# Performance work log

Measured on AMD Instinct MI355X. Metric: run time of the kernel, lower is better.

Reference implementation:

```python
import jax, jax.numpy as jnp
import numpy as np

N, E, F, H, C, B = 50000, 1_600_000, 128, 128, 10, 512


def setup_inputs() -> dict:
    key = jax.random.key(0)
    ks = jax.random.split(key, 12)
    inp = {
        "x": jax.random.normal(ks[0], (N, F), dtype=jnp.float32),
        "edge_index": jax.random.randint(ks[1], (2, E), 0, N, dtype=jnp.int32),
        "batch": jnp.sort(jax.random.randint(ks[2], (N,), 0, B, dtype=jnp.int32)),
        "edge_weight": jax.random.uniform(ks[3], (E,), dtype=jnp.float32),
        "W1": jax.random.normal(ks[4], (F, H), dtype=jnp.float32) * 0.05,
        "b1": jnp.zeros((H,), dtype=jnp.float32),
        "W2": jax.random.normal(ks[5], (H, H), dtype=jnp.float32) * 0.05,
        "b2": jnp.zeros((H,), dtype=jnp.float32),
        "W3": jax.random.normal(ks[6], (H, H), dtype=jnp.float32) * 0.05,
        "b3": jnp.zeros((H,), dtype=jnp.float32),
        "Wlin": jax.random.normal(ks[7], (H, C), dtype=jnp.float32) * 0.05,
        "blin": jnp.zeros((C,), dtype=jnp.float32),
    }
    return inp


def reference(x, edge_index, batch, edge_weight, W1, b1, W2, b2, W3, b3, Wlin, blin):
    n = x.shape[0]
    src, dst = edge_index[0], edge_index[1]
    loops = jnp.arange(n, dtype=src.dtype)
    src_f = jnp.concatenate([src, loops])  # edges + self-loops
    dst_f = jnp.concatenate([dst, loops])

    def make_norm(fill_value):
        # GCN symmetric normalization: D^-1/2 (A + fill*I) D^-1/2 on edge weights
        ew = jnp.concatenate([edge_weight, jnp.full((n,), fill_value, dtype=edge_weight.dtype)])
        deg = jax.ops.segment_sum(ew, dst_f, num_segments=n)
        dinv = jnp.where(deg > 0, deg ** -0.5, 0.0)
        return dinv[src_f] * ew * dinv[dst_f]

    # conv1 was built as GCNConv(in, hidden, out_channels) -> third positional arg is
    # `improved`, truthy => self-loop fill value 2.0; conv2/3 use 1.0.
    norm1 = make_norm(2.0)
    norm = make_norm(1.0)

    def gcn_conv(h, W, b, nrm):
        h = h @ W                                   # [N, H]
        msg = h[src_f] * nrm[:, None]               # [E+N, H] gather
        return jax.ops.segment_sum(msg, dst_f, num_segments=n) + b

    h = jax.nn.relu(gcn_conv(x, W1, b1, norm1))
    h = jax.nn.relu(gcn_conv(h, W2, b2, norm))
    h = gcn_conv(h, W3, b3, norm)

    # global_mean_pool over graph ids
    sums = jax.ops.segment_sum(h, batch, num_segments=B)
    cnt = jax.ops.segment_sum(jnp.ones((n,), dtype=h.dtype), batch, num_segments=B)
    pooled = sums / jnp.maximum(cnt, 1.0)[:, None]

    # dropout is identity in eval mode
    return pooled @ Wlin + blin
```

## Files before the change

### kernel.cpp

```cpp
#include <hip/hip_runtime.h>
#include <hip/hip_fp16.h>

#define F 128
#define HID 128
#define NCLS 10
#define CAP 80
#define NBIN 256
#define NPB 196
#define SCAP 7168
#define EPT 8
#define HLS 136

typedef short short8 __attribute__((ext_vector_type(8)));
typedef float float4v __attribute__((ext_vector_type(4)));
typedef float float2v __attribute__((ext_vector_type(2)));

__device__ __forceinline__ unsigned short f2bf(float f) {
    unsigned int u = __float_as_uint(f);
    unsigned int r = (u + 0x7FFFu + ((u >> 16) & 1u)) >> 16;
    return (unsigned short)r;
}
__device__ __forceinline__ float bf2f(unsigned int h) {
    return __uint_as_float(h << 16);
}
__device__ __forceinline__ unsigned char f2fp8(float a) {
    return (unsigned char)(__builtin_amdgcn_cvt_pk_fp8_f32(a, 0.f, 0, false) & 0xFF);
}

__global__ __launch_bounds__(256) void bin_prep_kernel(
    const int* __restrict__ ei, const float* __restrict__ ew,
    int* __restrict__ gcur, uint2* __restrict__ staging, int E, int nbb,
    const float* __restrict__ W1, const float* __restrict__ W2,
    const float* __restrict__ W3, const float* __restrict__ Wlin,
    const float* __restrict__ blin, const float* __restrict__ b3,
    unsigned short* __restrict__ Wp, unsigned short* __restrict__ Wp3s,
    float* __restrict__ bL) {
    __shared__ int lhist[NBIN];
    __shared__ int lscan[NBIN];
    __shared__ int lbase[NBIN];
    __shared__ uint2 lent[256 * EPT];
    int tid = threadIdx.x;

    if ((int)blockIdx.x < nbb) {
        lhist[tid] = 0;
        __syncthreads();

        unsigned int rpk[EPT];
        unsigned short rd[EPT];
        unsigned short rloc[EPT];
        int base = blockIdx.x * (256 * EPT);
#pragma unroll
        for (int i = 0; i < EPT; i++) {
            int e = base + tid + i * 256;
            if (e < E) {
                int s = ei[e];
                int d = ei[E + e];
                unsigned int q = (unsigned int)(ew[e] * 65535.0f + 0.5f);
                rpk[i] = (q << 16) | (unsigned int)s;
                rd[i] = (unsigned short)d;
                rloc[i] = (unsigned short)atomicAdd(&lhist[d / NPB], 1);
            } else {
                rpk[i] = 0u; rd[i] = 0; rloc[i] = 0xFFFF;
            }
        }
        __syncthreads();

        lscan[tid] = lhist[tid];
        __syncthreads();
        for (int off = 1; off < NBIN; off <<= 1) {
            int t = (tid >= off) ? lscan[tid - off] : 0;
            __syncthreads();
            lscan[tid] += t;
            __syncthreads();
        }
        lbase[tid] = atomicAdd(&gcur[tid], lhist[tid]);
        __syncthreads();

#pragma unroll
        for (int i = 0; i < EPT; i++) {
            if (rloc[i] != 0xFFFF) {
                int bin = (int)rd[i] / NPB;
                int slot = (lscan[bin] - lhist[bin]) + (int)rloc[i];
                lent[slot] = make_uint2(rpk[i], (unsigned int)rd[i]);
            }
        }
        __syncthreads();

        int total = lscan[NBIN - 1];
        for (int j = tid; j < total; j += 256) {
            uint2 t = lent[j];
            int bin = (int)t.y / NPB;
            int pos = lbase[bin] + (j - (lscan[bin] - lhist[bin]));
            if (pos < SCAP) staging[(size_t)bin * SCAP + pos] = t;
        }
    } else {
        int b = blockIdx.x - nbb;
        if (b < 128) {
            int widx = b >> 6;
            const float* W = (widx == 0) ? W1 : W2;
            int idx = (b & 63) * 256 + tid;
            int j = idx & 7;
            int l = (idx >> 3) & 63;
            int nt = (idx >> 9) & 7;
            int kt = idx >> 12;
            int k = kt * 32 + ((l >> 4) << 3) + j;
            int n = nt * 16 + (l & 15);
            Wp[widx * 16384 + idx] = f2bf(W[k * HID + n]);
        } else if (b < 136) {
            int idx = (b - 128) * 256 + tid;
            int j = idx & 7;
            int l = (idx >> 3) & 63;
            int kt = idx >> 9;
            int k = kt * 32 + ((l >> 4) << 3) + j;
            int n = l & 15;
            float v = 0.f;
            if (n < NCLS) {
                for (int m = 0; m < HID; m++)
                    v += W3[k * HID + m] * Wlin[m * NCLS + n];
            }
            Wp3s[idx] = f2bf(v);
        } else {
            if (tid < NCLS) {
                float bl = blin[tid];
                for (int j = 0; j < HID; j++) bl += b3[j] * Wlin[j * NCLS + tid];
                bL[tid] = bl;
            }
        }
    }
}

__global__ __launch_bounds__(1024, 8) void build_gemm1_kernel(
    const uint2* __restrict__ staging, const int* __restrict__ gcur,
    unsigned int* __restrict__ colw, int* __restrict__ cnt,
    float* __restrict__ dinv1, float* __restrict__ dinv0, int N, int nbins,
    const float* __restrict__ X, const unsigned short* __restrict__ Wp,
    unsigned char* __restrict__ Yb8) {
    __shared__ unsigned int lbuck[NPB * CAP];
    __shared__ int lcnt[NPB];
    int tid = threadIdx.x;

    if ((int)blockIdx.x < nbins) {
        int bin = blockIdx.x;
        int node0 = bin * NPB;

        for (int n = tid; n < NPB; n += 1024) lcnt[n] = 0;
        __syncthreads();

        int bcnt = gcur[bin];
        if (bcnt > SCAP) bcnt = SCAP;
        const uint2* st = staging + (size_t)bin * SCAP;
        for (int i = tid; i < bcnt; i += 1024) {
            uint2 t = st[i];
            int dl = (int)t.y - node0;
            int pos = atomicAdd(&lcnt[dl], 1);
            if (pos < CAP) lbuck[dl * CAP + pos] = t.x;
        }
        __syncthreads();

        for (int it = 0; it < NPB; it += 128) {
            int nl = it + (tid >> 3);
            int lane = tid & 7;
            if (nl < NPB) {
                int gn = node0 + nl;
                if (gn < N) {
                    int c = lcnt[nl];
                    if (c > CAP) c = CAP;
                    float s = 0.f;
                    for (int j = lane; j < c; j += 8)
                        s += (float)(lbuck[nl * CAP + j] >> 16);
                    s += __shfl_down(s, 4, 8);
                    s += __shfl_down(s, 2, 8);
                    s += __shfl_down(s, 1, 8);
                    if (lane == 0) {
                        float deg = s * (1.0f / 65535.0f);
                        cnt[gn] = c;
                        dinv1[gn] = 1.0f / sqrtf(deg + 2.0f);
                        dinv0[gn] = 1.0f / sqrtf(deg + 1.0f);
                    }
                }
            }
        }
        __syncthreads();

        int nvalid = N - node0;
        if (nvalid > NPB) nvalid = NPB;
        if (nvalid <= 0) return;
        int nslots = nvalid * (CAP / 4);
        uint4* dst4 = (uint4*)(colw + (size_t)node0 * CAP);
        const uint4* src4 = (const uint4*)lbuck;
        for (int i = tid; i < nslots; i += 1024) {
            int rowi = i / (CAP / 4);
            int slot = i - rowi * (CAP / 4);
            int c = lcnt[rowi];
            if (c > CAP) c = CAP;
            if (slot * 4 < c) dst4[i] = src4[i];
        }
    } else {
        int tile = blockIdx.x - nbins;
        int wave = tid >> 6, lane = tid & 63;
        int quad = lane >> 4, m = lane & 15;
        int row0 = tile * 256 + wave * 16;
        if (row0 >= N) return;
        int row = row0 + m;
        int rowc = row < N ? row : N - 1;

        short8 a[4];
        const float4* xrow = (const float4*)(X + (size_t)rowc * F);
#pragma unroll
        for (int kt = 0; kt < 4; kt++) {
            float4 p0 = xrow[kt * 8 + quad * 2];
            float4 p1 = xrow[kt * 8 + quad * 2 + 1];
            short8 v;
            v[0] = (short)f2bf(p0.x); v[1] = (short)f2bf(p0.y);
            v[2] = (short)f2bf(p0.z); v[3] = (short)f2bf(p0.w);
            v[4] = (short)f2bf(p1.x); v[5] = (short)f2bf(p1.y);
            v[6] = (short)f2bf(p1.z); v[7] = (short)f2bf(p1.w);
            a[kt] = v;
        }

#pragma unroll
        for (int nt = 0; nt < 8; nt++) {
            float4v c = {0.f, 0.f, 0.f, 0.f};
#pragma unroll
            for (int kt = 0; kt < 4; kt++) {
                short8 b = *(const short8*)(Wp + (((kt * 8 + nt) * 64 + lane) << 3));
                c = __builtin_amdgcn_mfma_f32_16x16x32_bf16(a[kt], b, c, 0, 0, 0);
            }
#pragma unroll
            for (int r = 0; r < 4; r++) {
                int gr = row0 + quad * 4 + r;
                if (gr < N) Yb8[(size_t)gr * HID + nt * 16 + m] = f2fp8(c[r]);
            }
        }
    }
}

__device__ __forceinline__ void agg_acc8(float f, const uint4& h,
                                         float2v acc[8]) {
    float2v fv = {f, f};
    acc[0] += fv * __builtin_amdgcn_cvt_pk_f32_fp8(h.x, false);
    acc[1] += fv * __builtin_amdgcn_cvt_pk_f32_fp8(h.x, true);
    acc[2] += fv * __builtin_amdgcn_cvt_pk_f32_fp8(h.y, false);
    acc[3] += fv * __builtin_amdgcn_cvt_pk_f32_fp8(h.y, true);
    acc[4] += fv * __builtin_amdgcn_cvt_pk_f32_fp8(h.z, false);
    acc[5] += fv * __builtin_amdgcn_cvt_pk_f32_fp8(h.z, true);
    acc[6] += fv * __builtin_amdgcn_cvt_pk_f32_fp8(h.w, false);
    acc[7] += fv * __builtin_amdgcn_cvt_pk_f32_fp8(h.w, true);
}

template <bool GD>
__device__ __forceinline__ void agg_b4(const unsigned int w[8], int t0, int fl,
                                       const uint4* __restrict__ hin4,
                                       const float* __restrict__ dinv,
                                       float2v acc[8]) {
    uint4 h[4];
    float dv[4];
#pragma unroll
    for (int t = 0; t < 4; t++) h[t] = hin4[(w[t0 + t] & 0xFFFFu) * 8 + fl];
    if (GD) {
#pragma unroll
        for (int t = 0; t < 4; t++) dv[t] = dinv[w[t0 + t] & 0xFFFFu];
    }
#pragma unroll
    for (int t = 0; t < 4; t++) {
        float f = (float)(w[t0 + t] >> 16) * (1.0f / 65535.0f);
        if (GD) f *= dv[t];
        agg_acc8(f, h[t], acc);
    }
}

template <bool GD>
__device__ __forceinline__ void agg_p32(unsigned int pk, int q, int fl,
                                        const uint4* __restrict__ hin4,
                                        const float* __restrict__ dinv,
                                        float2v acc[8]) {
    unsigned int w[8];
#pragma unroll
    for (int t = 0; t < 4; t++) {
        w[2 * t]     = (unsigned int)__shfl((int)pk, t * 8 + 2 * q, 32);
        w[2 * t + 1] = (unsigned int)__shfl((int)pk, t * 8 + 2 * q + 1, 32);
    }
    agg_b4<GD>(w, 0, fl, hin4, dinv, acc);
    agg_b4<GD>(w, 4, fl, hin4, dinv, acc);
}

template <bool GD>
__device__ __forceinline__ void agg_p8(unsigned int pk, int j0, int q, int fl,
                                       const uint4* __restrict__ hin4,
                                       const float* __restrict__ dinv,
                                       float2v acc[8]) {
    unsigned int w0 = (unsigned int)__shfl((int)pk, j0 + 2 * q, 32);
    unsigned int w1 = (unsigned int)__shfl((int)pk, j0 + 2 * q + 1, 32);
    uint4 h0 = hin4[(w0 & 0xFFFFu) * 8 + fl];
    uint4 h1 = hin4[(w1 & 0xFFFFu) * 8 + fl];
    float f0 = (float)(w0 >> 16) * (1.0f / 65535.0f);
    float f1 = (float)(w1 >> 16) * (1.0f / 65535.0f);
    if (GD) { f0 *= dinv[w0 & 0xFFFFu]; f1 *= dinv[w1 & 0xFFFFu]; }
    agg_acc8(f0, h0, acc);
    agg_acc8(f1, h1, acc);
}

template <bool GD>
__device__ __forceinline__ void agg_node_fp8(int g, int lane,
                                             const unsigned char* __restrict__ hin,
                                             const unsigned int* __restrict__ colw,
                                             const int* __restrict__ cnt,
                                             const float* __restrict__ dinv,
                                             float fill,
                                             const float* __restrict__ bias,
                                             unsigned short* __restrict__ hl_row) {
    float dv = dinv[g];
    int c = cnt[g];
    if (c > CAP) c = CAP;
    const unsigned int* row = colw + (size_t)g * CAP;
    const uint4* hin4 = (const uint4*)hin;

    unsigned int pk[3];
#pragma unroll
    for (int k = 0; k < 3; k++) {
        int idx = lane + k * 32;
        pk[k] = (idx < c) ? row[idx] : 0u;
    }

    int q = lane >> 3;
    int fl = lane & 7;

    float2v acc[8];
#pragma unroll
    for (int i = 0; i < 8; i++) acc[i] = (float2v){0.f, 0.f};

    agg_p32<GD>(pk[0], q, fl, hin4, dinv, acc);
    if (c > 32) {
        int cc = c - 32;
        if (cc > 32) cc = 32;
        for (int j = 0; j < cc; j += 8) agg_p8<GD>(pk[1], j, q, fl, hin4, dinv, acc);
    }
    if (c > 64) {
        int cc = c - 64;
        for (int j = 0; j < cc; j += 8) agg_p8<GD>(pk[2], j, q, fl, hin4, dinv, acc);
    }

#pragma unroll
    for (int i = 0; i < 8; i++) {
        acc[i][0] += __shfl_down(acc[i][0], 16, 32);
        acc[i][1] += __shfl_down(acc[i][1], 16, 32);
        acc[i][0] += __shfl_down(acc[i][0], 8, 32);
        acc[i][1] += __shfl_down(acc[i][1], 8, 32);
    }

    if (q == 0) {
        uint4 hv = hin4[(size_t)g * 8 + fl];
        float wsv = GD ? fill * dv : fill;
        float2v ws = {wsv, wsv};
        float2v dvv = {dv, dv};
        acc[0] = (acc[0] + ws * __builtin_amdgcn_cvt_pk_f32_fp8(hv.x, false)) * dvv;
        acc[1] = (acc[1] + ws * __builtin_amdgcn_cvt_pk_f32_fp8(hv.x, true)) * dvv;
        acc[2] = (acc[2] + ws * __builtin_amdgcn_cvt_pk_f32_fp8(hv.y, false)) * dvv;
        acc[3] = (acc[3] + ws * __builtin_amdgcn_cvt_pk_f32_fp8(hv.y, true)) * dvv;
        acc[4] = (acc[4] + ws * __builtin_amdgcn_cvt_pk_f32_fp8(hv.z, false)) * dvv;
        acc[5] = (acc[5] + ws * __builtin_amdgcn_cvt_pk_f32_fp8(hv.z, true)) * dvv;
        acc[6] = (acc[6] + ws * __builtin_amdgcn_cvt_pk_f32_fp8(hv.w, false)) * dvv;
        acc[7] = (acc[7] + ws * __builtin_amdgcn_cvt_pk_f32_fp8(hv.w, true)) * dvv;

        const float2v* b2 = (const float2v*)(bias + fl * 16);
        uint4 o0, o1;
        unsigned int ow[8];
#pragma unroll
        for (int i = 0; i < 8; i++) {
            float2v v = acc[i] + b2[i];
            float v0 = fmaxf(v[0], 0.f);
            float v1 = fmaxf(v[1], 0.f);
            ow[i] = (unsigned int)f2bf(v0) | ((unsigned int)f2bf(v1) << 16);
        }
        o0 = make_uint4(ow[0], ow[1], ow[2], ow[3]);
        o1 = make_uint4(ow[4], ow[5], ow[6], ow[7]);
        *(uint4*)(hl_row + fl * 16) = o0;
        *(uint4*)(hl_row + fl * 16 + 8) = o1;
    }
}

__global__ __launch_bounds__(512) void agg_gemm128_kernel(const unsigned char* __restrict__ hin,
                                                          const unsigned int* __restrict__ colw,
                                                          const int* __restrict__ cnt,
                                                          const float* __restrict__ dinv1,
                                                          const float* __restrict__ dinv0,
                                                          const float* __restrict__ bias,
                                                          const unsigned short* __restrict__ Wp2,
                                                          unsigned char* __restrict__ Yb8,
                                                          int N) {
    __shared__ unsigned short hl[16 * HLS];
    __shared__ unsigned char Ol8[16 * 128];

    int tid = threadIdx.x;
    int gl = tid >> 5, lane = tid & 31;
    int row0 = blockIdx.x * 16;
    int g = row0 + gl;

    if (g < N) {
        agg_node_fp8<true>(g, lane, hin, colw, cnt, dinv1, 2.0f, bias, hl + gl * HLS);
    } else if ((lane >> 3) == 0) {
        *(uint4*)(hl + gl * HLS + (lane & 7) * 16) = make_uint4(0u, 0u, 0u, 0u);
        *(uint4*)(hl + gl * HLS + (lane & 7) * 16 + 8) = make_uint4(0u, 0u, 0u, 0u);
    }
    __syncthreads();

    int nt = tid >> 6;
    int lane64 = tid & 63;
    int quad = lane64 >> 4, m = lane64 & 15;

    short8 a[4];
#pragma unroll
    for (int kt = 0; kt < 4; kt++)
        a[kt] = *(const short8*)(hl + m * HLS + kt * 32 + quad * 8);

    float4v c = {0.f, 0.f, 0.f, 0.f};
#pragma unroll
    for (int kt = 0; kt < 4; kt++) {
        short8 b = *(const short8*)(Wp2 + (((kt * 8 + nt) * 64 + lane64) << 3));
        c = __builtin_amdgcn_mfma_f32_16x16x32_bf16(a[kt], b, c, 0, 0, 0);
    }
#pragma unroll
    for (int r = 0; r < 4; r++) {
        int gr = row0 + quad * 4 + r;
        float sc = (gr < N) ? dinv0[gr] : 0.f;
        Ol8[(quad * 4 + r) * 128 + nt * 16 + m] = f2fp8(c[r] * sc);
    }
    __syncthreads();

    if (tid < 128) {
        int gr = row0 + (tid >> 3);
        if (gr < N)
            ((uint4*)(Yb8 + (size_t)gr * 128))[tid & 7] = ((const uint4*)Ol8)[tid];
    }
}

__global__ __launch_bounds__(512) void agg_gemm16_kernel(const unsigned char* __restrict__ hin,
                                                         const unsigned int* __restrict__ colw,
                                                         const int* __restrict__ cnt,
                                                         const float* __restrict__ dinv0,
                                                         const float* __restrict__ bias,
                                                         const unsigned short* __restrict__ Wp3s,
                                                         unsigned short* __restrict__ g3s,
                                                         int N) {
    __shared__ unsigned short hl[16 * HLS];

    int tid = threadIdx.x;
    int gl = tid >> 5, lane = tid & 31;
    int row0 = blockIdx.x * 16;
    int g = row0 + gl;

    if (g < N) {
        agg_node_fp8<false>(g, lane, hin, colw, cnt, dinv0, 1.0f, bias, hl + gl * HLS);
    } else if ((lane >> 3) == 0) {
        *(uint4*)(hl + gl * HLS + (lane & 7) * 16) = make_uint4(0u, 0u, 0u, 0u);
        *(uint4*)(hl + gl * HLS + (lane & 7) * 16 + 8) = make_uint4(0u, 0u, 0u, 0u);
    }
    __syncthreads();

    if (tid < 64) {
        int lane64 = tid;
        int quad = lane64 >> 4, m = lane64 & 15;
        short8 a[4];
#pragma unroll
        for (int kt = 0; kt < 4; kt++)
            a[kt] = *(const short8*)(hl + m * HLS + kt * 32 + quad * 8);
        float4v c = {0.f, 0.f, 0.f, 0.f};
#pragma unroll
        for (int kt = 0; kt < 4; kt++) {
            short8 b = *(const short8*)(Wp3s + ((kt * 64 + lane64) << 3));
            c = __builtin_amdgcn_mfma_f32_16x16x32_bf16(a[kt], b, c, 0, 0, 0);
        }
#pragma unroll
        for (int r = 0; r < 4; r++) {
            int gr = row0 + quad * 4 + r;
            if (gr < N)
                g3s[(size_t)gr * 16 + m] = f2bf(c[r] * dinv0[gr]);
        }
    }
}

__device__ __forceinline__ void agg3_slot(unsigned int pk, int lane2off,
                                          const unsigned short* __restrict__ g3s,
                                          float& ax, float& ay) {
    unsigned int w[8];
    unsigned int h[8];
#pragma unroll
    for (int t = 0; t < 8; t++)
        w[t] = (unsigned int)__shfl((int)pk, t, 8);
#pragma unroll
    for (int t = 0; t < 8; t++)
        h[t] = *(const unsigned int*)(g3s + (w[t] & 0xFFFFu) * 16 + lane2off);
#pragma unroll
    for (int t = 0; t < 8; t++) {
        float f = (float)(w[t] >> 16) * (1.0f / 65535.0f);
        ax += f * bf2f(h[t] & 0xFFFFu);
        ay += f * bf2f(h[t] >> 16);
    }
}

__global__ __launch_bounds__(256) void agg3_kernel(const unsigned short* __restrict__ g3s,
                                                   const unsigned int* __restrict__ colw,
                                                   const int* __restrict__ cnt,
                                                   const float* __restrict__ dinv0,
                                                   unsigned short* __restrict__ h3s, int N) {
    int g = (blockIdx.x * blockDim.x + threadIdx.x) >> 3;
    int lane = threadIdx.x & 7;
    if (g >= N) return;

    float dv = dinv0[g];
    int c = cnt[g];
    if (c > CAP) c = CAP;
    const unsigned int* row = colw + (size_t)g * CAP;
    int lane2off = lane * 2;

    unsigned int pk[10];
#pragma unroll
    for (int k = 0; k < 10; k++) {
        int idx = lane + k * 8;
        pk[k] = (idx < c) ? row[idx] : 0u;
    }

    float ax = 0.f, ay = 0.f;
#pragma unroll
    for (int slot = 0; slot < 10; slot++) {
        int base = slot * 8;
        if (c > base) agg3_slot(pk[slot], lane2off, g3s, ax, ay);
    }

    unsigned int hv = *(const unsigned int*)(g3s + (size_t)g * 16 + lane2off);
    ax = (ax + bf2f(hv & 0xFFFFu)) * dv;
    ay = (ay + bf2f(hv >> 16)) * dv;

    unsigned int o = (unsigned int)f2bf(ax) | ((unsigned int)f2bf(ay) << 16);
    *(unsigned int*)(h3s + (size_t)g * 16 + lane2off) = o;
}

__global__ __launch_bounds__(256) void pool3_kernel(const unsigned short* __restrict__ h3s,
                                                    const int* __restrict__ batch,
                                                    const float* __restrict__ bL,
                                                    const float* __restrict__ blin,
                                                    float* __restrict__ out, int N, int B) {
    int wave = (blockIdx.x * blockDim.x + threadIdx.x) >> 6;
    int lane = threadIdx.x & 63;
    if (wave >= B) return;
    int g = wave;
    int d = lane & 15, sub = lane >> 4;

    int lo = 0, hi = N;
    while (lo < hi) { int m = (lo + hi) >> 1; if (batch[m] < g) lo = m + 1; else hi = m; }
    int s0 = lo;
    hi = N;
    while (lo < hi) { int m = (lo + hi) >> 1; if (batch[m] < g + 1) lo = m + 1; else hi = m; }
    int s1 = lo;

    float p = 0.f;
    for (int v = s0 + sub; v < s1; v += 4)
        p += bf2f((unsigned int)h3s[(size_t)v * 16 + d]);
    p += __shfl_down(p, 32, 64);
    p += __shfl_down(p, 16, 64);

    if (lane < NCLS) {
        int cntv = s1 - s0;
        float r = (cntv > 0) ? (p / (float)cntv + bL[d]) : blin[d];
        out[g * NCLS + d] = r;
    }
}

extern "C" void kernel_launch(void* const* d_in, const int* in_sizes, int n_in,
                              void* d_out, int out_size, void* d_ws, size_t ws_size,
                              hipStream_t stream) {
    const float* x    = (const float*)d_in[0];
    const int*   ei   = (const int*)d_in[1];
    const int*   batch= (const int*)d_in[2];
    const float* ew   = (const float*)d_in[3];
    const float* W1   = (const float*)d_in[4];
    const float* b1   = (const float*)d_in[5];
    const float* W2   = (const float*)d_in[6];
    const float* b2   = (const float*)d_in[7];
    const float* W3   = (const float*)d_in[8];
    const float* b3   = (const float*)d_in[9];
    const float* Wlin = (const float*)d_in[10];
    const float* blin = (const float*)d_in[11];
    float* out = (float*)d_out;

    int N = in_sizes[0] / F;
    int E = in_sizes[1] / 2;
    int B = out_size / NCLS;

    char* p = (char*)d_ws;
    auto alloc = [&](size_t bytes) -> void* {
        void* r = (void*)p;
        p += (bytes + 255) & ~(size_t)255;
        return r;
    };
    int*            cnt   = (int*)alloc((size_t)N * 4);
    float*          dinv1 = (float*)alloc((size_t)N * 4);
    float*          dinv0 = (float*)alloc((size_t)N * 4);
    int*            gcur  = (int*)alloc(NBIN * 4);
    float*          bL    = (float*)alloc(16 * 4);
    unsigned int*   colw  = (unsigned int*)alloc((size_t)N * CAP * 4);
    unsigned short* Wp    = (unsigned short*)alloc(2 * 16384 * 2);
    unsigned short* Wp3s  = (unsigned short*)alloc(2048 * 2);
    unsigned char*  bufA  = (unsigned char*)alloc((size_t)N * HID);
    unsigned char*  bufB  = (unsigned char*)alloc((size_t)N * HID);
    unsigned short* g3s   = (unsigned short*)alloc((size_t)N * 16 * 2);
    unsigned short* h3s   = (unsigned short*)alloc((size_t)N * 16 * 2);
    uint2*          staging = (uint2*)alloc((size_t)NBIN * SCAP * 8);

    int tb = 256;
    int nbins = (N + NPB - 1) / NPB;
    int nbb = (E + tb * EPT - 1) / (tb * EPT);
    int g1tiles = (N + 255) / 256;

    hipMemsetAsync(gcur, 0, NBIN * 4, stream);
    bin_prep_kernel<<<nbb + 137, tb, 0, stream>>>(ei, ew, gcur, staging, E, nbb,
                                                  W1, W2, W3, Wlin, blin, b3,
                                                  Wp, Wp3s, bL);
    build_gemm1_kernel<<<nbins + g1tiles, 1024, 0, stream>>>(staging, gcur, colw, cnt,
                                                             dinv1, dinv0, N, nbins,
                                                             x, Wp, bufA);

    int fused_blocks = (N + 15) / 16;
    int agg3_blocks = ((N * 8) + tb - 1) / tb;

    agg_gemm128_kernel<<<fused_blocks, 512, 0, stream>>>(bufA, colw, cnt, dinv1, dinv0,
                                                         b1, Wp + 16384, bufB, N);
    agg_gemm16_kernel<<<fused_blocks, 512, 0, stream>>>(bufB, colw, cnt, dinv0, b2,
                                                        Wp3s, g3s, N);
    agg3_kernel<<<agg3_blocks, tb, 0, stream>>>(g3s, colw, cnt, dinv0, h3s, N);
    pool3_kernel<<<((B * 64) + tb - 1) / tb, tb, 0, stream>>>(h3s, batch, bL, blin,
                                                              out, N, B);
}
```

Measured before the change: 231.8 us.

## Fuse layer-3 aggregation with mean pooling via atomics and last-block finalize

Measured after the change: 407.1 us. 1.76x slower.

```diff
diff --git a/kernel.cpp b/kernel.cpp
--- a/kernel.cpp
+++ b/kernel.cpp
@@ -10,6 +10,7 @@
 #define SCAP 7168
 #define EPT 8
 #define HLS 136
+#define GSPAN 34
 
 typedef short short8 __attribute__((ext_vector_type(8)));
 typedef float float4v __attribute__((ext_vector_type(4)));
@@ -498,71 +499,92 @@
     }
 }
 
-__global__ __launch_bounds__(256) void agg3_kernel(const unsigned short* __restrict__ g3s,
-                                                   const unsigned int* __restrict__ colw,
-                                                   const int* __restrict__ cnt,
-                                                   const float* __restrict__ dinv0,
-                                                   unsigned short* __restrict__ h3s, int N) {
-    int g = (blockIdx.x * blockDim.x + threadIdx.x) >> 3;
-    int lane = threadIdx.x & 7;
-    if (g >= N) return;
-
-    float dv = dinv0[g];
-    int c = cnt[g];
-    if (c > CAP) c = CAP;
-    const unsigned int* row = colw + (size_t)g * CAP;
+__global__ __launch_bounds__(256) void agg3_pool_kernel(
+    const unsigned short* __restrict__ g3s,
+    const unsigned int* __restrict__ colw, const int* __restrict__ cnt,
+    const float* __restrict__ dinv0, const int* __restrict__ batch,
+    const float* __restrict__ bL, const float* __restrict__ blin,
+    float* __restrict__ psum, unsigned int* __restrict__ done,
+    float* __restrict__ out, int N, int B) {
+    __shared__ float lsum[GSPAN * 16];
+    __shared__ int lbg0;
+    __shared__ bool amLast;
+    int tid = threadIdx.x;
+
+    for (int i = tid; i < GSPAN * 16; i += 256) lsum[i] = 0.f;
+    if (tid == 0) lbg0 = batch[blockIdx.x * 32];
+    __syncthreads();
+    int bg0 = lbg0;
+
+    int g = blockIdx.x * 32 + (tid >> 3);
+    int lane = tid & 7;
     int lane2off = lane * 2;
 
-    unsigned int pk[10];
-#pragma unroll
-    for (int k = 0; k < 10; k++) {
-        int idx = lane + k * 8;
-        pk[k] = (idx < c) ? row[idx] : 0u;
-    }
-
-    float ax = 0.f, ay = 0.f;
-#pragma unroll
-    for (int slot = 0; slot < 10; slot++) {
-        int base = slot * 8;
-        if (c > base) agg3_slot(pk[slot], lane2off, g3s, ax, ay);
-    }
-
-    unsigned int hv = *(const unsigned int*)(g3s + (size_t)g * 16 + lane2off);
-    ax = (ax + bf2f(hv & 0xFFFFu)) * dv;
-    ay = (ay + bf2f(hv >> 16)) * dv;
-
-    unsigned int o = (unsigned int)f2bf(ax) | ((unsigned int)f2bf(ay) << 16);
-    *(unsigned int*)(h3s + (size_t)g * 16 + lane2off) = o;
-}
-
-__global__ __launch_bounds__(256) void pool3_kernel(const unsigned short* __restrict__ h3s,
-                                                    const int* __restrict__ batch,
-                                                    const float* __restrict__ bL,
-                                                    const float* __restrict__ blin,
-                                                    float* __restrict__ out, int N, int B) {
-    int wave = (blockIdx.x * blockDim.x + threadIdx.x) >> 6;
-    int lane = threadIdx.x & 63;
-    if (wave >= B) return;
-    int g = wave;
-    int d = lane & 15, sub = lane >> 4;
-
-    int lo = 0, hi = N;
-    while (lo < hi) { int m = (lo + hi) >> 1; if (batch[m] < g) lo = m + 1; else hi = m; }
-    int s0 = lo;
-    hi = N;
-    while (lo < hi) { int m = (lo + hi) >> 1; if (batch[m] < g + 1) lo = m + 1; else hi = m; }
-    int s1 = lo;
-
-    float p = 0.f;
-    for (int v = s0 + sub; v < s1; v += 4)
-        p += bf2f((unsigned int)h3s[(size_t)v * 16 + d]);
-    p += __shfl_down(p, 32, 64);
-    p += __shfl_down(p, 16, 64);
-
-    if (lane < NCLS) {
-        int cntv = s1 - s0;
-        float r = (cntv > 0) ? (p / (float)cntv + bL[d]) : blin[d];
-        out[g * NCLS + d] = r;
+    if (g < N) {
+        float dv = dinv0[g];
+        int c = cnt[g];
+        if (c > CAP) c = CAP;
+        const unsigned int* row = colw + (size_t)g * CAP;
+
+        unsigned int pk[10];
+#pragma unroll
+        for (int k = 0; k < 10; k++) {
+            int idx = lane + k * 8;
+            pk[k] = (idx < c) ? row[idx] : 0u;
+        }
+
+        float ax = 0.f, ay = 0.f;
+#pragma unroll
+        for (int slot = 0; slot < 10; slot++) {
+            if (c > slot * 8) agg3_slot(pk[slot], lane2off, g3s, ax, ay);
+        }
+
+        unsigned int hv = *(const unsigned int*)(g3s + (size_t)g * 16 + lane2off);
+        ax = (ax + bf2f(hv & 0xFFFFu)) * dv;
+        ay = (ay + bf2f(hv >> 16)) * dv;
+
+        int bg = batch[g];
+        int o = bg - bg0;
+        if (o >= 0 && o < GSPAN) {
+            atomicAdd(&lsum[o * 16 + lane2off], ax);
+            atomicAdd(&lsum[o * 16 + lane2off + 1], ay);
+        } else {
+            atomicAdd(&psum[bg * 16 + lane2off], ax);
+            atomicAdd(&psum[bg * 16 + lane2off + 1], ay);
+        }
+    }
+    __syncthreads();
+
+    for (int i = tid; i < GSPAN * 16; i += 256) {
+        float v = lsum[i];
+        if (v != 0.f) {
+            int bg = bg0 + (i >> 4);
+            if (bg < B) atomicAdd(&psum[bg * 16 + (i & 15)], v);
+        }
+    }
+    __syncthreads();
+
+    if (tid == 0) {
+        __threadfence();
+        unsigned int old = atomicAdd(done, 1u);
+        amLast = (old == gridDim.x - 1);
+    }
+    __syncthreads();
+
+    if (amLast) {
+        __threadfence();
+        for (int i = tid; i < B * 16; i += 256) {
+            int gg = i >> 4, d = i & 15;
+            if (d >= NCLS) continue;
+            int lo = 0, hi = N;
+            while (lo < hi) { int m = (lo + hi) >> 1; if (batch[m] < gg) lo = m + 1; else hi = m; }
+            int s0 = lo;
+            hi = N;
+            while (lo < hi) { int m = (lo + hi) >> 1; if (batch[m] < gg + 1) lo = m + 1; else hi = m; }
+            int cntv = lo - s0;
+            out[gg * NCLS + d] = (cntv > 0) ? (psum[i] / (float)cntv + bL[d])
+                                            : blin[d];
+        }
     }
 }
 
@@ -597,6 +619,8 @@
     float*          dinv1 = (float*)alloc((size_t)N * 4);
     float*          dinv0 = (float*)alloc((size_t)N * 4);
     int*            gcur  = (int*)alloc(NBIN * 4);
+    unsigned int*   done  = (unsigned int*)alloc(4);
+    float*          psum  = (float*)alloc((size_t)B * 16 * 4);
     float*          bL    = (float*)alloc(16 * 4);
     unsigned int*   colw  = (unsigned int*)alloc((size_t)N * CAP * 4);
     unsigned short* Wp    = (unsigned short*)alloc(2 * 16384 * 2);
@@ -604,7 +628,6 @@
     unsigned char*  bufA  = (unsigned char*)alloc((size_t)N * HID);
     unsigned char*  bufB  = (unsigned char*)alloc((size_t)N * HID);
     unsigned short* g3s   = (unsigned short*)alloc((size_t)N * 16 * 2);
-    unsigned short* h3s   = (unsigned short*)alloc((size_t)N * 16 * 2);
     uint2*          staging = (uint2*)alloc((size_t)NBIN * SCAP * 8);
 
     int tb = 256;
@@ -612,7 +635,8 @@
     int nbb = (E + tb * EPT - 1) / (tb * EPT);
     int g1tiles = (N + 255) / 256;
 
-    hipMemsetAsync(gcur, 0, NBIN * 4, stream);
+    size_t zlen = (size_t)NBIN * 4 + 256 + ((size_t)B * 16 * 4 + 255 & ~(size_t)255);
+    hipMemsetAsync(gcur, 0, zlen, stream);
     bin_prep_kernel<<<nbb + 137, tb, 0, stream>>>(ei, ew, gcur, staging, E, nbb,
                                                   W1, W2, W3, Wlin, blin, b3,
                                                   Wp, Wp3s, bL);
@@ -621,13 +645,12 @@
                                                              x, Wp, bufA);
 
     int fused_blocks = (N + 15) / 16;
-    int agg3_blocks = ((N * 8) + tb - 1) / tb;
+    int a3p_blocks = (N + 31) / 32;
 
     agg_gemm128_kernel<<<fused_blocks, 512, 0, stream>>>(bufA, colw, cnt, dinv1, dinv0,
                                                          b1, Wp + 16384, bufB, N);
     agg_gemm16_kernel<<<fused_blocks, 512, 0, stream>>>(bufB, colw, cnt, dinv0, b2,
                                                         Wp3s, g3s, N);
-    agg3_kernel<<<agg3_blocks, tb, 0, stream>>>(g3s, colw, cnt, dinv0, h3s, N);
-    pool3_kernel<<<((B * 64) + tb - 1) / tb, tb, 0, stream>>>(h3s, batch, bL, blin,
-                                                              out, N, B);
-}
+    agg3_pool_kernel<<<a3p_blocks, tb, 0, stream>>>(g3s, colw, cnt, dinv0, batch,
+                                                    bL, blin, psum, done, out, N, B);
+}
```
